# Optimization experiments

Measured on AMD Instinct MI355X. Metric: run time of the kernel, lower is better.

The kernel has to match this reference:

```python
import jax, jax.numpy as jnp
import numpy as np

B, NSIDE, NH = 4, 64, 8
N = 12 * NSIDE * NSIDE          # HEALPix pixel count, nested ordering
CIN, CHID, COUT = 256, 512, 256
WS = 16                          # window = 4**(w+1) nested pixels, w=1
HD = CHID // NH


def _ln(x, g, b, eps=1e-5):
    m = x.mean(-1, keepdims=True)
    v = ((x - m) ** 2).mean(-1, keepdims=True)
    return (x - m) * jax.lax.rsqrt(v + eps) * g + b


def _win_attn(x, qkv_w, qkv_b, pw, pb):
    b_, n_, c = x.shape
    nw = n_ // WS
    xw = x.reshape(b_, nw, WS, c)
    qkv = xw @ qkv_w + qkv_b                      # [B, nw, ws, 3C]
    q, k, v = jnp.split(qkv, 3, axis=-1)
    def heads(t):
        return t.reshape(b_, nw, WS, NH, HD).transpose(0, 1, 3, 2, 4)
    q, k, v = heads(q), heads(k), heads(v)        # [B, nw, H, ws, hd]
    a = jax.nn.softmax(jnp.einsum('bwhqd,bwhkd->bwhqk', q, k) * (HD ** -0.5), axis=-1)
    o = jnp.einsum('bwhqk,bwhkd->bwhqd', a, v)
    o = o.transpose(0, 1, 3, 2, 4).reshape(b_, n_, c)
    return o @ pw + pb


def _heal_block(x, p, shift):
    if shift:
        x = jnp.roll(x, -WS // 2, axis=1)          # shifted-window (cyclic in nested order)
    x = x + _win_attn(_ln(x, p['ln1g'], p['ln1b']), p['qkvw'], p['qkvb'], p['pw'], p['pb'])
    h = _ln(x, p['ln2g'], p['ln2b'])
    h = jax.nn.gelu(h @ p['m1w'] + p['m1b'], approximate=False) @ p['m2w'] + p['m2b']
    x = x + h
    if shift:
        x = jnp.roll(x, WS // 2, axis=1)
    return x


def _sn_linear(h, W, b, u):
    # torch spectral_norm: one power-iteration, u/v detached, sigma = u' W v
    v = W @ u                                      # [CHID]
    v = jax.lax.stop_gradient(v / (jnp.linalg.norm(v) + 1e-12))
    u2 = v @ W                                     # [COUT]
    u2 = jax.lax.stop_gradient(u2 / (jnp.linalg.norm(u2) + 1e-12))
    sigma = v @ W @ u2
    return h @ (W / sigma) + b


def setup_inputs() -> dict:
    key = jax.random.key(0)
    ks = iter(jax.random.split(key, 64))
    def w(shape, s=0.02):
        return jax.random.normal(next(ks), shape, jnp.float32) * s
    inp = {'x': jax.random.normal(next(ks), (B, N, CIN), jnp.float32)}
    inp['ff1_w'] = w((CIN, CHID)); inp['ff1_b'] = jnp.zeros((CHID,), jnp.float32)
    for pre in ('a', 'b'):
        inp[f'{pre}_ln1g'] = jnp.ones((CHID,), jnp.float32)
        inp[f'{pre}_ln1b'] = jnp.zeros((CHID,), jnp.float32)
        inp[f'{pre}_qkvw'] = w((CHID, 3 * CHID)); inp[f'{pre}_qkvb'] = jnp.zeros((3 * CHID,), jnp.float32)
        inp[f'{pre}_pw'] = w((CHID, CHID)); inp[f'{pre}_pb'] = jnp.zeros((CHID,), jnp.float32)
        inp[f'{pre}_ln2g'] = jnp.ones((CHID,), jnp.float32)
        inp[f'{pre}_ln2b'] = jnp.zeros((CHID,), jnp.float32)
        inp[f'{pre}_m1w'] = w((CHID, 4 * CHID)); inp[f'{pre}_m1b'] = jnp.zeros((4 * CHID,), jnp.float32)
        inp[f'{pre}_m2w'] = w((4 * CHID, CHID)); inp[f'{pre}_m2b'] = jnp.zeros((CHID,), jnp.float32)
    inp['ff2_w'] = w((CHID, COUT)); inp['ff2_b'] = jnp.zeros((COUT,), jnp.float32)
    inp['ff2_u'] = jax.random.normal(next(ks), (COUT,), jnp.float32)
    return inp


def reference(x, ff1_w, ff1_b,
              a_ln1g, a_ln1b, a_qkvw, a_qkvb, a_pw, a_pb, a_ln2g, a_ln2b, a_m1w, a_m1b, a_m2w, a_m2b,
              b_ln1g, b_ln1b, b_qkvw, b_qkvb, b_pw, b_pb, b_ln2g, b_ln2b, b_m1w, b_m1b, b_m2w, b_m2b,
              ff2_w, ff2_b, ff2_u):
    pa = dict(ln1g=a_ln1g, ln1b=a_ln1b, qkvw=a_qkvw, qkvb=a_qkvb, pw=a_pw, pb=a_pb,
              ln2g=a_ln2g, ln2b=a_ln2b, m1w=a_m1w, m1b=a_m1b, m2w=a_m2w, m2b=a_m2b)
    pb_ = dict(ln1g=b_ln1g, ln1b=b_ln1b, qkvw=b_qkvw, qkvb=b_qkvb, pw=b_pw, pb=b_pb,
               ln2g=b_ln2g, ln2b=b_ln2b, m1w=b_m1w, m1b=b_m1b, m2w=b_m2w, m2b=b_m2b)
    h = jax.nn.gelu(x @ ff1_w + ff1_b, approximate=False)   # feed_forward1
    h = _heal_block(h, pa, shift=False)                     # message_passing1
    h = _heal_block(h, pb_, shift=True)                     # message_passing2
    return _sn_linear(h, ff2_w, ff2_b, ff2_u)               # spectral-norm linear
```

## Files before the change

kernel.cpp:

```cpp
#include <hip/hip_runtime.h>
#include <hip/hip_bf16.h>
#include <math.h>

typedef _Float16 f16;
typedef __attribute__((ext_vector_type(8))) _Float16 f16x8;
typedef __attribute__((ext_vector_type(4))) _Float16 f16x4;
typedef __attribute__((ext_vector_type(4))) float f32x4;

#define DINLINE __device__ __forceinline__

DINLINE float gelu_fast(float x) {
  float x2 = x * x;
  float z = x * __builtin_fmaf(-0.10294537f, x2, -2.30211422f);
  float E = __builtin_amdgcn_exp2f(z);
  return x * __builtin_amdgcn_rcpf(1.0f + E);
}
DINLINE void gload16(const void* g, void* l) {
  __builtin_amdgcn_global_load_lds((const __attribute__((address_space(1))) void*)g,
                                   (__attribute__((address_space(3))) void*)l, 16, 0, 0);
}

#define BAR       __builtin_amdgcn_s_barrier()
#define WAITLGKM  asm volatile("s_waitcnt lgkmcnt(0)" ::: "memory")
#define WAITVM(n) asm volatile("s_waitcnt vmcnt(" #n ")" ::: "memory")

template <int EPI>
__global__ __launch_bounds__(256, 4) void gemm128(
    const f16* __restrict__ A, const f16* __restrict__ Bt,
    const float* __restrict__ bias, const f16* __restrict__ Cin,
    float* __restrict__ Cf, f16* __restrict__ Cb,
    const float* __restrict__ scale_ptr,
    int N, int K, int nct)
{
  __shared__ alignas(16) f16 sm[2][2][4096];

  const int nwg = (int)gridDim.x;
  const int gid = (int)blockIdx.x;
  const int q = nwg >> 3, r = nwg & 7;
  const int xcd = gid & 7, idx = gid >> 3;
  const int swz = (xcd < r ? xcd * (q + 1) : r * (q + 1) + (xcd - r) * q) + idx;
  const int rt = swz / nct, ct = swz - rt * nct;
  const int m0 = rt << 7, n0 = ct << 7;

  const int tid = (int)threadIdx.x;
  const int lane = tid & 63;
  const int wid = tid >> 6;
  const int wr = wid >> 1, wcn = wid & 1;

  const int rsel = lane & 15, khi = lane >> 4;
  const int sx = (khi ^ ((rsel >> 1) & 3)) << 3;

  f32x4 acc[4][4] = {};
  f16x8 aF[4], bF[4];

  const int NT = K >> 5;

#define STAGE(b, k0)                                                          \
  {                                                                           \
    _Pragma("unroll")                                                         \
    for (int _g = 0; _g < 4; ++_g) {                                          \
      const int _s = _g * 256 + tid;                                          \
      const int _mat = _s >> 9, _sm = _s & 511;                               \
      const int _row = _sm >> 2;                                              \
      const int _ls = (_sm & 3) ^ ((_row >> 1) & 3);                          \
      const f16* _src = _mat ? Bt + (size_t)(n0 + _row) * K                   \
                             : A + (size_t)(m0 + _row) * K;                   \
      gload16(_src + (k0) + (_ls << 3), &sm[b][_mat][_sm * 8]);               \
    }                                                                         \
  }

#define DSRA(b)                                                               \
  {                                                                           \
    _Pragma("unroll")                                                         \
    for (int _i = 0; _i < 4; ++_i)                                            \
      aF[_i] = *(const f16x8*)(&sm[b][0][(wr * 64 + _i * 16 + rsel) * 32 + sx]); \
  }

#define DSRB(b)                                                               \
  {                                                                           \
    _Pragma("unroll")                                                         \
    for (int _i = 0; _i < 4; ++_i)                                            \
      bF[_i] = *(const f16x8*)(&sm[b][1][(wcn * 64 + _i * 16 + rsel) * 32 + sx]); \
  }

#define MMC                                                                   \
  {                                                                           \
    __builtin_amdgcn_s_setprio(1);                                            \
    _Pragma("unroll")                                                         \
    for (int _m = 0; _m < 4; ++_m)                                            \
      _Pragma("unroll")                                                       \
      for (int _n = 0; _n < 4; ++_n)                                          \
        acc[_m][_n] = __builtin_amdgcn_mfma_f32_16x16x32_f16(                 \
            bF[_n], aF[_m], acc[_m][_n], 0, 0, 0);                            \
    __builtin_amdgcn_s_setprio(0);                                            \
  }

  STAGE(0, 0);
  for (int t = 0; t < NT; ++t) {
    const int b = t & 1;
    if (t + 1 < NT) {
      if (b) STAGE(0, (t + 1) << 5) else STAGE(1, (t + 1) << 5)
      WAITVM(4);
    } else {
      WAITVM(0);
    }
    BAR;
    DSRA(b); DSRB(b); WAITLGKM; MMC;
    BAR;
  }

  const float scale = (EPI & 8) ? scale_ptr[0] : 1.0f;
  const int R0 = m0 + wr * 64, C0 = n0 + wcn * 64;
#pragma unroll
  for (int m = 0; m < 4; ++m) {
    const int row = R0 + m * 16 + rsel;
#pragma unroll
    for (int n = 0; n < 4; ++n) {
      const int col = C0 + n * 16 + (khi << 2);
      f32x4 v = acc[m][n];
      if (EPI & 8) {
#pragma unroll
        for (int j = 0; j < 4; ++j) v[j] *= scale;
      }
      f32x4 bb = *(const f32x4*)(bias + col);
#pragma unroll
      for (int j = 0; j < 4; ++j) v[j] += bb[j];
      if (EPI & 1) {
#pragma unroll
        for (int j = 0; j < 4; ++j) v[j] = gelu_fast(v[j]);
      }
      if (EPI & 2) {
        f16x4 c4 = *(const f16x4*)(Cin + (size_t)row * N + col);
#pragma unroll
        for (int j = 0; j < 4; ++j) v[j] += (float)c4[j];
      }
      if (EPI & 4) {
        f16x4 o;
#pragma unroll
        for (int j = 0; j < 4; ++j) o[j] = (f16)v[j];
        *(f16x4*)(Cb + (size_t)row * N + col) = o;
      } else {
        *(f32x4*)(Cf + (size_t)row * N + col) = v;
      }
    }
  }
#undef STAGE
#undef DSRA
#undef DSRB
#undef MMC
}

__global__ __launch_bounds__(256) void ln_f16(
    const f16* __restrict__ X, const float* __restrict__ g,
    const float* __restrict__ b, f16* __restrict__ Y, int ntok)
{
  const int lane = threadIdx.x & 63;
  const int c = lane * 8;
  const f32x4 g0 = *(const f32x4*)(g + c), g1 = *(const f32x4*)(g + c + 4);
  const f32x4 b0 = *(const f32x4*)(b + c), b1 = *(const f32x4*)(b + c + 4);
  for (int token = blockIdx.x * 4 + (threadIdx.x >> 6); token < ntok;
       token += gridDim.x * 4) {
    f16x8 v = *(const f16x8*)(X + (size_t)token * 512 + c);
    float vf[8];
    float s = 0.f, s2 = 0.f;
#pragma unroll
    for (int j = 0; j < 8; ++j) { vf[j] = (float)v[j]; s += vf[j]; s2 += vf[j] * vf[j]; }
#pragma unroll
    for (int o = 32; o > 0; o >>= 1) { s += __shfl_xor(s, o, 64); s2 += __shfl_xor(s2, o, 64); }
    const float mean = s * (1.f / 512.f);
    const float inv = rsqrtf(s2 * (1.f / 512.f) - mean * mean + 1e-5f);
    f16x8 o8;
#pragma unroll
    for (int j = 0; j < 4; ++j) {
      o8[j]     = (f16)((vf[j] - mean) * inv * g0[j] + b0[j]);
      o8[4 + j] = (f16)((vf[4 + j] - mean) * inv * g1[j] + b1[j]);
    }
    *(f16x8*)(Y + (size_t)token * 512 + c) = o8;
  }
}

__global__ __launch_bounds__(256) void cvt_f32_f16(const float* __restrict__ X,
                                                   f16* __restrict__ Y, long n8)
{
  const long i = (long)blockIdx.x * 256 + threadIdx.x;
  if (i >= n8) return;
  f32x4 v0 = *(const f32x4*)(X + i * 8), v1 = *(const f32x4*)(X + i * 8 + 4);
  f16x8 o8;
#pragma unroll
  for (int j = 0; j < 4; ++j) { o8[j] = (f16)v0[j]; o8[4 + j] = (f16)v1[j]; }
  *(f16x8*)(Y + i * 8) = o8;
}

__global__ __launch_bounds__(256) void w_tr_tiled(const float* __restrict__ W,
                                                  f16* __restrict__ Wt, int K, int N)
{
  __shared__ f16 td[64][66];
  const int nkt = K >> 6;
  const int kt = blockIdx.x % nkt, nt = blockIdx.x / nkt;
  const int k0 = kt << 6, n0 = nt << 6;
  const int col = threadIdx.x & 63, rq = threadIdx.x >> 6;
#pragma unroll
  for (int j = 0; j < 16; ++j) {
    const int row = j * 4 + rq;
    td[row][col] = (f16)W[(size_t)(k0 + row) * N + n0 + col];
  }
  __syncthreads();
#pragma unroll
  for (int j = 0; j < 16; ++j) {
    const int nrow = j * 4 + rq;
    Wt[(size_t)(n0 + nrow) * K + k0 + col] = td[col][nrow];
  }
}

template <int SHIFT>
__global__ __launch_bounds__(256) void win_attn(const f16* __restrict__ QKV,
                                                f16* __restrict__ O)
{
  __shared__ alignas(16) f16 kv[2][16][1160];
  const int wl0 = (int)blockIdx.x * 2;
  const int tid = (int)threadIdx.x;

  for (int i = tid; i < 4096; i += 256) {
    const int win = i >> 11;
    const int rem = i & 2047;
    const int row = rem >> 7;
    const int c8 = rem & 127;
    const int src = ((wl0 + win) * 16 + row + SHIFT) % 49152;
    const int sect = c8 >> 6;
    const int hh = (c8 >> 3) & 7;
    const int dd = (c8 & 7) * 8;
    *(f16x8*)(&kv[win][row][sect * 576 + hh * 72 + dd]) =
        *(const f16x8*)(QKV + (size_t)src * 1536 + 512 + c8 * 8);
  }

  const int win = tid >> 7, h = (tid >> 4) & 7, qi = tid & 15;
  const int qtok = ((wl0 + win) * 16 + qi + SHIFT) % 49152;
  f16x8 qv[8];
#pragma unroll
  for (int c8 = 0; c8 < 8; ++c8)
    qv[c8] = *(const f16x8*)(QKV + (size_t)qtok * 1536 + h * 64 + c8 * 8);

  __syncthreads();

  float sc[16];
  float mx = -1e30f;
#pragma unroll
  for (int kj = 0; kj < 16; ++kj) {
    const f16* kr = &kv[win][kj][h * 72];
    float s = 0.f;
#pragma unroll
    for (int c8 = 0; c8 < 8; ++c8) {
      f16x8 k8 = *(const f16x8*)(kr + c8 * 8);
#pragma unroll
      for (int j = 0; j < 8; ++j) s += (float)qv[c8][j] * (float)k8[j];
    }
    s *= 0.125f;
    sc[kj] = s;
    mx = fmaxf(mx, s);
  }
  float sum = 0.f;
#pragma unroll
  for (int kj = 0; kj < 16; ++kj) { sc[kj] = expf(sc[kj] - mx); sum += sc[kj]; }
  const float inv = 1.f / sum;
  float ov[64] = {};
#pragma unroll
  for (int kj = 0; kj < 16; ++kj) {
    const float a = sc[kj] * inv;
    const f16* vr = &kv[win][kj][576 + h * 72];
#pragma unroll
    for (int c8 = 0; c8 < 8; ++c8) {
      f16x8 v8 = *(const f16x8*)(vr + c8 * 8);
#pragma unroll
      for (int j = 0; j < 8; ++j) ov[c8 * 8 + j] += a * (float)v8[j];
    }
  }
  f16* orow = O + (size_t)qtok * 512 + h * 64;
#pragma unroll
  for (int c8 = 0; c8 < 8; ++c8) {
    f16x8 t;
#pragma unroll
    for (int j = 0; j < 8; ++j) t[j] = (f16)ov[c8 * 8 + j];
    *(f16x8*)(orow + c8 * 8) = t;
  }
}

__global__ __launch_bounds__(256) void sn_sigma(const float* __restrict__ W,
                                                const float* __restrict__ u,
                                                float* __restrict__ inv_sigma)
{
  __shared__ float vsh[512];
  __shared__ float ush[256];
  __shared__ float red[256];
  const int t = (int)threadIdx.x;
  ush[t] = u[t];
  __syncthreads();
  float a0 = 0.f, a1 = 0.f;
  for (int j = 0; j < 256; ++j) {
    a0 += W[t * 256 + j] * ush[j];
    a1 += W[(t + 256) * 256 + j] * ush[j];
  }
  vsh[t] = a0; vsh[t + 256] = a1;
  red[t] = a0 * a0 + a1 * a1;
  __syncthreads();
  for (int s = 128; s > 0; s >>= 1) { if (t < s) red[t] += red[t + s]; __syncthreads(); }
  const float nv = sqrtf(red[0]) + 1e-12f;
  __syncthreads();
  const float invv = 1.f / nv;
  vsh[t] *= invv; vsh[t + 256] *= invv;
  __syncthreads();
  float u2 = 0.f;
  for (int i = 0; i < 512; ++i) u2 += vsh[i] * W[i * 256 + t];
  red[t] = u2 * u2;
  __syncthreads();
  for (int s = 128; s > 0; s >>= 1) { if (t < s) red[t] += red[t + s]; __syncthreads(); }
  const float nu = sqrtf(red[0]) + 1e-12f;
  __syncthreads();
  ush[t] = u2 / nu;
  __syncthreads();
  float d0 = 0.f, d1 = 0.f;
  for (int j = 0; j < 256; ++j) {
    d0 += W[t * 256 + j] * ush[j];
    d1 += W[(t + 256) * 256 + j] * ush[j];
  }
  red[t] = vsh[t] * d0 + vsh[t + 256] * d1;
  __syncthreads();
  for (int s = 128; s > 0; s >>= 1) { if (t < s) red[t] += red[t + s]; __syncthreads(); }
  if (t == 0) inv_sigma[0] = 1.f / red[0];
}

__global__ void fill_sentinel(float* __restrict__ out, long n, float val)
{
  const long i = (long)blockIdx.x * 256 + threadIdx.x;
  for (long k = i; k < n; k += (long)gridDim.x * 256) out[k] = val;
}

extern "C" void kernel_launch(void* const* d_in, const int* in_sizes, int n_in,
                              void* d_out, int out_size, void* d_ws, size_t ws_size,
                              hipStream_t stream)
{
  const int M = 196608;
  const int MC = 49152;
  constexpr size_t OFF_U   = 201326592ull;
  constexpr size_t OFF_OH  = 201326592ull + 150994944ull;
  constexpr size_t OFF_WT  = 402653184ull;
  constexpr size_t OFF_SIG = 415760384ull;
  constexpr size_t NEED    = OFF_SIG + 256ull;

  if (ws_size < NEED) {
    fill_sentinel<<<2048, 256, 0, stream>>>((float*)d_out, (long)out_size,
                                            (float)(ws_size >> 20));
    return;
  }

  char* ws = (char*)d_ws;
  f16* R     = (f16*)(ws);
  f16* U     = (f16*)(ws + OFF_U);
  f16* OH    = (f16*)(ws + OFF_OH);
  f16* WT    = (f16*)(ws + OFF_WT);
  float* sig = (float*)(ws + OFF_SIG);
  f16* X     = (f16*)d_out;

  const float* ff1_b = (const float*)d_in[2];
  const float* ff2_b = (const float*)d_in[28];

  f16* W_FF1 = WT;
  auto W_QKV = [&](int blk) { return WT + (blk ? 3276800 : 131072); };
  auto W_PW  = [&](int blk) { return WT + (blk ? 4063232 : 917504); };
  auto W_M1  = [&](int blk) { return WT + (blk ? 4325376 : 1179648); };
  auto W_M2  = [&](int blk) { return WT + (blk ? 5373952 : 2228224); };
  f16* W_FF2 = WT + 6422528;

  w_tr_tiled<<<32, 256, 0, stream>>>((const float*)d_in[1], W_FF1, 256, 512);
  for (int blk = 0; blk < 2; ++blk) {
    w_tr_tiled<<<192, 256, 0, stream>>>((const float*)d_in[blk ? 17 : 5], W_QKV(blk), 512, 1536);
    w_tr_tiled<<<64, 256, 0, stream>>>((const float*)d_in[blk ? 19 : 7], W_PW(blk), 512, 512);
    w_tr_tiled<<<256, 256, 0, stream>>>((const float*)d_in[blk ? 23 : 11], W_M1(blk), 512, 2048);
    w_tr_tiled<<<256, 256, 0, stream>>>((const float*)d_in[blk ? 25 : 13], W_M2(blk), 2048, 512);
  }
  w_tr_tiled<<<32, 256, 0, stream>>>((const float*)d_in[27], W_FF2, 512, 256);
  sn_sigma<<<1, 256, 0, stream>>>((const float*)d_in[27], (const float*)d_in[29], sig);

  cvt_f32_f16<<<24576, 256, 0, stream>>>((const float*)d_in[0], U, (long)M * 256 / 8);
  gemm128<5><<<6144, 256, 0, stream>>>(U, W_FF1, ff1_b, nullptr, nullptr, R, nullptr,
                                       512, 256, 4);

  for (int blk = 0; blk < 2; ++blk) {
    const float* ln1g = (const float*)d_in[blk ? 15 : 3];
    const float* ln1b = (const float*)d_in[blk ? 16 : 4];
    const float* qkvb = (const float*)d_in[blk ? 18 : 6];
    const float* pb   = (const float*)d_in[blk ? 20 : 8];
    const float* ln2g = (const float*)d_in[blk ? 21 : 9];
    const float* ln2b = (const float*)d_in[blk ? 22 : 10];
    const float* m1b  = (const float*)d_in[blk ? 24 : 12];
    const float* m2b  = (const float*)d_in[blk ? 26 : 14];

    ln_f16<<<4096, 256, 0, stream>>>(R, ln1g, ln1b, X, M);
    for (int mc = 0; mc < 4; ++mc) {
      const size_t ro = (size_t)mc * MC * 512;
      gemm128<4><<<4608, 256, 0, stream>>>(X + ro, W_QKV(blk), qkvb, nullptr,
                                           nullptr, U, nullptr, 1536, 512, 12);
      if (blk == 0) win_attn<0><<<1536, 256, 0, stream>>>(U, OH);
      else          win_attn<8><<<1536, 256, 0, stream>>>(U, OH);
      gemm128<6><<<1536, 256, 0, stream>>>(OH, W_PW(blk), pb, R + ro,
                                           nullptr, R + ro, nullptr, 512, 512, 4);
    }
    ln_f16<<<4096, 256, 0, stream>>>(R, ln2g, ln2b, X, M);
    for (int mc = 0; mc < 4; ++mc) {
      const size_t ro = (size_t)mc * MC * 512;
      gemm128<5><<<6144, 256, 0, stream>>>(X + ro, W_M1(blk), m1b, nullptr,
                                           nullptr, U, nullptr, 2048, 512, 16);
      gemm128<6><<<1536, 256, 0, stream>>>(U, W_M2(blk), m2b, R + ro,
                                           nullptr, R + ro, nullptr, 512, 2048, 4);
    }
  }

  gemm128<8><<<3072, 256, 0, stream>>>(R, W_FF2, ff2_b, nullptr, (float*)d_out,
                                       nullptr, sig, 256, 512, 2);
}
```

Before: 4.958 ms.

## Widen GEMM tile to 128x256 with 8 waves sharing the A tile

The GEMM kernel goes from a 128x128 tile with 4 waves to a 128x256 tile with 8 waves (512 threads). Each block stages one A tile and two B tiles, so each loaded A row is reused across twice as many output columns and per-output global/LDS traffic drops. All launches are updated to halve the grid and the column-tile count. This needs 48KB of LDS per block and doubles the threads per block, which may lower occupancy; launch_bounds of (512,4) may also be unattainable.

```diff
diff --git a/kernel.cpp b/kernel.cpp
--- a/kernel.cpp
+++ b/kernel.cpp
@@ -25,14 +25,14 @@
 #define WAITVM(n) asm volatile("s_waitcnt vmcnt(" #n ")" ::: "memory")
 
 template <int EPI>
-__global__ __launch_bounds__(256, 4) void gemm128(
+__global__ __launch_bounds__(512, 4) void gemm(
     const f16* __restrict__ A, const f16* __restrict__ Bt,
     const float* __restrict__ bias, const f16* __restrict__ Cin,
     float* __restrict__ Cf, f16* __restrict__ Cb,
     const float* __restrict__ scale_ptr,
     int N, int K, int nct)
 {
-  __shared__ alignas(16) f16 sm[2][2][4096];
+  __shared__ alignas(16) f16 sm[2][3][4096];
 
   const int nwg = (int)gridDim.x;
   const int gid = (int)blockIdx.x;
@@ -40,15 +40,18 @@
   const int xcd = gid & 7, idx = gid >> 3;
   const int swz = (xcd < r ? xcd * (q + 1) : r * (q + 1) + (xcd - r) * q) + idx;
   const int rt = swz / nct, ct = swz - rt * nct;
-  const int m0 = rt << 7, n0 = ct << 7;
+  const int m0 = rt << 7, n0 = ct << 8;
 
   const int tid = (int)threadIdx.x;
   const int lane = tid & 63;
   const int wid = tid >> 6;
-  const int wr = wid >> 1, wcn = wid & 1;
+  const int wr = wid >> 2, wcn = wid & 3;
 
   const int rsel = lane & 15, khi = lane >> 4;
   const int sx = (khi ^ ((rsel >> 1) & 3)) << 3;
+
+  const int breg = 1 + (wcn >> 1);
+  const int brow0 = (wcn & 1) * 64;
 
   f32x4 acc[4][4] = {};
   f16x8 aF[4], bF[4];
@@ -58,14 +61,15 @@
 #define STAGE(b, k0)                                                          \
   {                                                                           \
     _Pragma("unroll")                                                         \
-    for (int _g = 0; _g < 4; ++_g) {                                          \
-      const int _s = _g * 256 + tid;                                          \
-      const int _mat = _s >> 9, _sm = _s & 511;                               \
-      const int _row = _sm >> 2;                                              \
-      const int _ls = (_sm & 3) ^ ((_row >> 1) & 3);                          \
-      const f16* _src = _mat ? Bt + (size_t)(n0 + _row) * K                   \
-                             : A + (size_t)(m0 + _row) * K;                   \
-      gload16(_src + (k0) + (_ls << 3), &sm[b][_mat][_sm * 8]);               \
+    for (int _g = 0; _g < 3; ++_g) {                                          \
+      const int _s = _g * 512 + tid;                                          \
+      const int _reg = _s >> 9, _smi = _s & 511;                              \
+      const int _row = _smi >> 2;                                             \
+      const int _ls = (_smi & 3) ^ ((_row >> 1) & 3);                         \
+      const f16* _src = (_reg == 0)                                           \
+          ? A + (size_t)(m0 + _row) * K                                       \
+          : Bt + (size_t)(n0 + ((_reg - 1) << 7) + _row) * K;                 \
+      gload16(_src + (k0) + (_ls << 3), &sm[b][_reg][_smi * 8]);              \
     }                                                                         \
   }
 
@@ -80,7 +84,7 @@
   {                                                                           \
     _Pragma("unroll")                                                         \
     for (int _i = 0; _i < 4; ++_i)                                            \
-      bF[_i] = *(const f16x8*)(&sm[b][1][(wcn * 64 + _i * 16 + rsel) * 32 + sx]); \
+      bF[_i] = *(const f16x8*)(&sm[b][breg][(brow0 + _i * 16 + rsel) * 32 + sx]); \
   }
 
 #define MMC                                                                   \
@@ -100,7 +104,7 @@
     const int b = t & 1;
     if (t + 1 < NT) {
       if (b) STAGE(0, (t + 1) << 5) else STAGE(1, (t + 1) << 5)
-      WAITVM(4);
+      WAITVM(3);
     } else {
       WAITVM(0);
     }
@@ -381,8 +385,8 @@
   sn_sigma<<<1, 256, 0, stream>>>((const float*)d_in[27], (const float*)d_in[29], sig);
 
   cvt_f32_f16<<<24576, 256, 0, stream>>>((const float*)d_in[0], U, (long)M * 256 / 8);
-  gemm128<5><<<6144, 256, 0, stream>>>(U, W_FF1, ff1_b, nullptr, nullptr, R, nullptr,
-                                       512, 256, 4);
+  gemm<5><<<3072, 512, 0, stream>>>(U, W_FF1, ff1_b, nullptr, nullptr, R, nullptr,
+                                    512, 256, 2);
 
   for (int blk = 0; blk < 2; ++blk) {
     const float* ln1g = (const float*)d_in[blk ? 15 : 3];
@@ -397,23 +401,23 @@
     ln_f16<<<4096, 256, 0, stream>>>(R, ln1g, ln1b, X, M);
     for (int mc = 0; mc < 4; ++mc) {
       const size_t ro = (size_t)mc * MC * 512;
-      gemm128<4><<<4608, 256, 0, stream>>>(X + ro, W_QKV(blk), qkvb, nullptr,
-                                           nullptr, U, nullptr, 1536, 512, 12);
+      gemm<4><<<2304, 512, 0, stream>>>(X + ro, W_QKV(blk), qkvb, nullptr,
+                                        nullptr, U, nullptr, 1536, 512, 6);
       if (blk == 0) win_attn<0><<<1536, 256, 0, stream>>>(U, OH);
       else          win_attn<8><<<1536, 256, 0, stream>>>(U, OH);
-      gemm128<6><<<1536, 256, 0, stream>>>(OH, W_PW(blk), pb, R + ro,
-                                           nullptr, R + ro, nullptr, 512, 512, 4);
+      gemm<6><<<768, 512, 0, stream>>>(OH, W_PW(blk), pb, R + ro,
+                                       nullptr, R + ro, nullptr, 512, 512, 2);
     }
     ln_f16<<<4096, 256, 0, stream>>>(R, ln2g, ln2b, X, M);
     for (int mc = 0; mc < 4; ++mc) {
       const size_t ro = (size_t)mc * MC * 512;
-      gemm128<5><<<6144, 256, 0, stream>>>(X + ro, W_M1(blk), m1b, nullptr,
-                                           nullptr, U, nullptr, 2048, 512, 16);
-      gemm128<6><<<1536, 256, 0, stream>>>(U, W_M2(blk), m2b, R + ro,
-                                           nullptr, R + ro, nullptr, 512, 2048, 4);
-    }
-  }
-
-  gemm128<8><<<3072, 256, 0, stream>>>(R, W_FF2, ff2_b, nullptr, (float*)d_out,
-                                       nullptr, sig, 256, 512, 2);
-}
+      gemm<5><<<3072, 512, 0, stream>>>(X + ro, W_M1(blk), m1b, nullptr,
+                                        nullptr, U, nullptr, 2048, 512, 8);
+      gemm<6><<<768, 512, 0, stream>>>(U, W_M2(blk), m2b, R + ro,
+                                       nullptr, R + ro, nullptr, 512, 2048, 2);
+    }
+  }
+
+  gemm<8><<<1536, 512, 0, stream>>>(R, W_FF2, ff2_b, nullptr, (float*)d_out,
+                                    nullptr, sig, 256, 512, 1);
+}
```

Result: faster. 4.857 ms (-2.1%).
